# Performance work log

Hardware: AMD Instinct MI355X
Metric: run time of the kernel (lower is better)

## Reference

```python
import jax, jax.numpy as jnp
import numpy as np

B, G, CIN, COUT = 1024, 64, 512, 512  # G = s**(num_layers-1) = 2**6


def setup_inputs() -> dict:
    key = jax.random.key(0)
    kx, kw = jax.random.split(key)
    x = jax.random.normal(kx, (B, G, CIN), dtype=jnp.float32)
    weight = jax.random.normal(kw, (G, CIN, COUT), dtype=jnp.float32)
    return {"x": x, "weight": weight}


def reference(x, weight):
    # Original: (x[:,:,:,None] * W[None]).sum(2) / sqrt(Cin), then sum over groups.
    # Fused equivalent: grouped contraction over (g, c) -> [B, Cout].
    scale = 1.0 / jnp.sqrt(jnp.asarray(x.shape[2], dtype=x.dtype))
    out = jnp.einsum("bgc,gco->bo", x, weight) * scale
    return out
```

## Files before the change

kernel.cpp:

```cpp
#include <hip/hip_runtime.h>
#include <hip/hip_bf16.h>

typedef __bf16 bf16x8 __attribute__((ext_vector_type(8)));
typedef __bf16 bf16x4 __attribute__((ext_vector_type(4)));
typedef float  f32x4  __attribute__((ext_vector_type(4)));

#define B_SZ    1024
#define COUT_SZ 512
#define K_SZ    32768
#define TM 256
#define TN 256
#define BK 32

__device__ __forceinline__ void async_copy16(const void* g, void* l) {
  __builtin_amdgcn_global_load_lds(
      (const __attribute__((address_space(1))) unsigned int*)g,
      (__attribute__((address_space(3))) unsigned int*)l, 16, 0, 0);
}

__global__ __launch_bounds__(256) void wtrans_kernel(
    const float* __restrict__ w, __bf16* __restrict__ wt) {
  __shared__ float t[64 * 65];
  const int kb = blockIdx.x * 64;
  const int ob = blockIdx.y * 64;
  const int tid = threadIdx.x;

  {
    const int o4 = (tid & 15) * 4;
    const int kr = tid >> 4;
    const float* src = w + (size_t)(kb + kr) * COUT_SZ + ob + o4;
#pragma unroll
    for (int i = 0; i < 4; ++i) {
      f32x4 v = *(const f32x4*)(src + (size_t)(16 * i) * COUT_SZ);
      *(f32x4*)&t[(kr + 16 * i) * 65 + o4] = v;
    }
  }
  __syncthreads();
  {
    const int k4 = (tid & 15) * 4;
    const int orow = tid >> 4;
#pragma unroll
    for (int j = 0; j < 4; ++j) {
      const int o = orow + 16 * j;
      bf16x4 p;
#pragma unroll
      for (int e = 0; e < 4; ++e) p[e] = (__bf16)t[(k4 + e) * 65 + o];
      *(bf16x4*)(wt + (size_t)(ob + o) * K_SZ + kb + k4) = p;
    }
  }
}

__global__ __launch_bounds__(512, 2)
void gemm_kernel(const float* __restrict__ x, const __bf16* __restrict__ wt,
                 float* __restrict__ dst, int kchunk, int S) {
  __shared__ float  Asm[2][TM * BK];
  __shared__ __bf16 Bsm[2][TN * BK];

  const int lin = blockIdx.x;
  const int z = lin % S;
  const int t = lin / S;
  const int m0 = (t & 3) * TM;
  const int n0 = (t >> 2) * TN;
  const int tid  = threadIdx.x;
  const int w    = tid >> 6;
  const int lane = tid & 63;

  const int kbase = z * kchunk;

  const int aRow = lane >> 3;
  const int aCh  = (lane & 7) ^ aRow;
  const float* ag0 = x + (size_t)(m0 + (w * 4 + 0) * 8 + aRow) * K_SZ + kbase + aCh * 4;
  const float* ag1 = x + (size_t)(m0 + (w * 4 + 1) * 8 + aRow) * K_SZ + kbase + aCh * 4;
  const float* ag2 = x + (size_t)(m0 + (w * 4 + 2) * 8 + aRow) * K_SZ + kbase + aCh * 4;
  const float* ag3 = x + (size_t)(m0 + (w * 4 + 3) * 8 + aRow) * K_SZ + kbase + aCh * 4;
  const int bRow = lane >> 2;
  const int bCh  = (lane & 3) ^ ((lane >> 3) & 3);
  const __bf16* bg0 = wt + (size_t)(n0 + (w * 2 + 0) * 16 + bRow) * K_SZ + kbase + bCh * 8;
  const __bf16* bg1 = wt + (size_t)(n0 + (w * 2 + 1) * 16 + bRow) * K_SZ + kbase + bCh * 8;

  const int lm = lane & 15;
  const int q  = lane >> 4;
  const int wm = (w & 1) * 128;
  const int wn = (w >> 1) * 64;
  const int aPcLo = (2 * q) ^ (lm & 7);
  const int bPc   = q ^ ((lm >> 1) & 3);

  f32x4 acc[8][4];
#pragma unroll
  for (int i = 0; i < 8; ++i)
#pragma unroll
    for (int j = 0; j < 4; ++j)
      acc[i][j] = (f32x4){0.f, 0.f, 0.f, 0.f};

  async_copy16(ag0, &Asm[0][(w * 4 + 0) * 256]);
  async_copy16(ag1, &Asm[0][(w * 4 + 1) * 256]);
  async_copy16(ag2, &Asm[0][(w * 4 + 2) * 256]);
  async_copy16(ag3, &Asm[0][(w * 4 + 3) * 256]);
  async_copy16(bg0, &Bsm[0][(w * 2 + 0) * 512]);
  async_copy16(bg1, &Bsm[0][(w * 2 + 1) * 512]);
  ag0 += BK; ag1 += BK; ag2 += BK; ag3 += BK; bg0 += BK; bg1 += BK;

  const int niter = kchunk / BK;
  for (int it = 0; it < niter; ++it) {
    __syncthreads();
    const int p = it & 1;
    if (it + 1 < niter) {
      const int np = p ^ 1;
      async_copy16(ag0, &Asm[np][(w * 4 + 0) * 256]);
      async_copy16(ag1, &Asm[np][(w * 4 + 1) * 256]);
      async_copy16(ag2, &Asm[np][(w * 4 + 2) * 256]);
      async_copy16(ag3, &Asm[np][(w * 4 + 3) * 256]);
      async_copy16(bg0, &Bsm[np][(w * 2 + 0) * 512]);
      async_copy16(bg1, &Bsm[np][(w * 2 + 1) * 512]);
      ag0 += BK; ag1 += BK; ag2 += BK; ag3 += BK; bg0 += BK; bg1 += BK;
    }

    const float*  A_ = Asm[p];
    const __bf16* B_ = Bsm[p];
    bf16x8 bfr[4];
#pragma unroll
    for (int j = 0; j < 4; ++j)
      bfr[j] = *(const bf16x8*)&B_[(wn + j * 16 + lm) * BK + bPc * 8];

#pragma unroll
    for (int i = 0; i < 8; ++i) {
      const float* rowp = &A_[(wm + i * 16 + lm) * BK];
      f32x4 lo = *(const f32x4*)(rowp + aPcLo * 4);
      f32x4 hi = *(const f32x4*)(rowp + (aPcLo ^ 1) * 4);
      bf16x8 a;
#pragma unroll
      for (int e = 0; e < 4; ++e) {
        a[e]     = (__bf16)lo[e];
        a[e + 4] = (__bf16)hi[e];
      }
#pragma unroll
      for (int j = 0; j < 4; ++j)
        acc[i][j] = __builtin_amdgcn_mfma_f32_16x16x32_bf16(a, bfr[j], acc[i][j], 0, 0, 0);
    }
  }

  float* outp = dst + (size_t)z * (B_SZ * COUT_SZ)
              + (size_t)(m0 + wm + q * 4) * COUT_SZ + (n0 + wn + lm);
#pragma unroll
  for (int i = 0; i < 8; ++i) {
#pragma unroll
    for (int r = 0; r < 4; ++r) {
      float* o2 = outp + (size_t)(i * 16 + r) * COUT_SZ;
#pragma unroll
      for (int j = 0; j < 4; ++j)
        o2[j * 16] = acc[i][j][r];
    }
  }
}

__global__ __launch_bounds__(256) void reduce_kernel(
    const float* __restrict__ p, float* __restrict__ out, int S, float scale) {
  const int i = (blockIdx.x * 256 + threadIdx.x) * 4;
  f32x4 s0 = (f32x4){0.f, 0.f, 0.f, 0.f};
  f32x4 s1 = (f32x4){0.f, 0.f, 0.f, 0.f};
  int zz = 0;
  for (; zz + 1 < S; zz += 2) {
    s0 = s0 + *(const f32x4*)(p + (size_t)zz * (B_SZ * COUT_SZ) + i);
    s1 = s1 + *(const f32x4*)(p + (size_t)(zz + 1) * (B_SZ * COUT_SZ) + i);
  }
  for (; zz < S; ++zz)
    s0 = s0 + *(const f32x4*)(p + (size_t)zz * (B_SZ * COUT_SZ) + i);
  s0 = (s0 + s1) * scale;
  *(f32x4*)(out + i) = s0;
}

extern "C" void kernel_launch(void* const* d_in, const int* in_sizes, int n_in,
                              void* d_out, int out_size, void* d_ws, size_t ws_size,
                              hipStream_t stream) {
  const float* x = (const float*)d_in[0];
  const float* w = (const float*)d_in[1];
  float* out = (float*)d_out;

  const size_t wtB    = (size_t)COUT_SZ * K_SZ * sizeof(__bf16);
  const size_t sliceB = (size_t)B_SZ * COUT_SZ * sizeof(float);

  __bf16* wt = (__bf16*)d_ws;
  int S = 32;
  while (S > 1 && wtB + (size_t)S * sliceB > ws_size) S >>= 1;
  float* partials = (float*)((char*)d_ws + wtB);

  const float scale = 0.04419417382415922f;

  hipLaunchKernelGGL(wtrans_kernel, dim3(K_SZ / 64, COUT_SZ / 64), dim3(256), 0,
                     stream, w, wt);
  hipLaunchKernelGGL(gemm_kernel, dim3(8 * S), dim3(512), 0, stream,
                     x, wt, partials, K_SZ / S, S);
  hipLaunchKernelGGL(reduce_kernel, dim3(B_SZ * COUT_SZ / 1024), dim3(256), 0,
                     stream, partials, out, S, scale);
}
```

Baseline: 302.2 us.

## Pre-convert x to bf16 and use smaller single-buffered GEMM tiles

```diff
diff --git a/kernel.cpp b/kernel.cpp
--- a/kernel.cpp
+++ b/kernel.cpp
@@ -8,8 +8,8 @@
 #define B_SZ    1024
 #define COUT_SZ 512
 #define K_SZ    32768
-#define TM 256
-#define TN 256
+#define TM 128
+#define TN 128
 #define BK 32
 
 __device__ __forceinline__ void async_copy16(const void* g, void* l) {
@@ -18,13 +18,30 @@
       (__attribute__((address_space(3))) unsigned int*)l, 16, 0, 0);
 }
 
-__global__ __launch_bounds__(256) void wtrans_kernel(
+#define XCVT_BLOCKS 16384
+
+__global__ __launch_bounds__(256) void prep_kernel(
+    const float* __restrict__ x, __bf16* __restrict__ xb,
     const float* __restrict__ w, __bf16* __restrict__ wt) {
   __shared__ float t[64 * 65];
-  const int kb = blockIdx.x * 64;
-  const int ob = blockIdx.y * 64;
+  int b = blockIdx.x;
+  if (b < XCVT_BLOCKS) {
+    const size_t i = ((size_t)b * 256 + threadIdx.x) * 8;
+    f32x4 a = *(const f32x4*)(x + i);
+    f32x4 c = *(const f32x4*)(x + i + 4);
+    bf16x8 o;
+#pragma unroll
+    for (int e = 0; e < 4; ++e) {
+      o[e]     = (__bf16)a[e];
+      o[e + 4] = (__bf16)c[e];
+    }
+    *(bf16x8*)(xb + i) = o;
+    return;
+  }
+  b -= XCVT_BLOCKS;
+  const int kb = (b & 511) * 64;
+  const int ob = (b >> 9) * 64;
   const int tid = threadIdx.x;
-
   {
     const int o4 = (tid & 15) * 4;
     const int kr = tid >> 4;
@@ -50,99 +67,76 @@
   }
 }
 
-__global__ __launch_bounds__(512, 2)
-void gemm_kernel(const float* __restrict__ x, const __bf16* __restrict__ wt,
+__global__ __launch_bounds__(256, 3)
+void gemm_kernel(const __bf16* __restrict__ xb, const __bf16* __restrict__ wt,
                  float* __restrict__ dst, int kchunk, int S) {
-  __shared__ float  Asm[2][TM * BK];
-  __shared__ __bf16 Bsm[2][TN * BK];
+  __shared__ __bf16 As[TM * BK];
+  __shared__ __bf16 Bs[TN * BK];
 
   const int lin = blockIdx.x;
   const int z = lin % S;
   const int t = lin / S;
-  const int m0 = (t & 3) * TM;
-  const int n0 = (t >> 2) * TN;
+  const int m0 = (t & 7) * TM;
+  const int n0 = (t >> 3) * TN;
   const int tid  = threadIdx.x;
   const int w    = tid >> 6;
   const int lane = tid & 63;
-
   const int kbase = z * kchunk;
 
-  const int aRow = lane >> 3;
-  const int aCh  = (lane & 7) ^ aRow;
-  const float* ag0 = x + (size_t)(m0 + (w * 4 + 0) * 8 + aRow) * K_SZ + kbase + aCh * 4;
-  const float* ag1 = x + (size_t)(m0 + (w * 4 + 1) * 8 + aRow) * K_SZ + kbase + aCh * 4;
-  const float* ag2 = x + (size_t)(m0 + (w * 4 + 2) * 8 + aRow) * K_SZ + kbase + aCh * 4;
-  const float* ag3 = x + (size_t)(m0 + (w * 4 + 3) * 8 + aRow) * K_SZ + kbase + aCh * 4;
-  const int bRow = lane >> 2;
-  const int bCh  = (lane & 3) ^ ((lane >> 3) & 3);
-  const __bf16* bg0 = wt + (size_t)(n0 + (w * 2 + 0) * 16 + bRow) * K_SZ + kbase + bCh * 8;
-  const __bf16* bg1 = wt + (size_t)(n0 + (w * 2 + 1) * 16 + bRow) * K_SZ + kbase + bCh * 8;
+  const int sRow = lane >> 2;
+  const int sCh  = (lane & 3) ^ (sRow & 3);
+  const __bf16* ag0 = xb + (size_t)(m0 + w * 32 + sRow) * K_SZ + kbase + sCh * 8;
+  const __bf16* ag1 = xb + (size_t)(m0 + w * 32 + 16 + sRow) * K_SZ + kbase + sCh * 8;
+  const __bf16* bg0 = wt + (size_t)(n0 + w * 32 + sRow) * K_SZ + kbase + sCh * 8;
+  const __bf16* bg1 = wt + (size_t)(n0 + w * 32 + 16 + sRow) * K_SZ + kbase + sCh * 8;
+  __bf16* aL0 = &As[(w * 32) * BK];
+  __bf16* aL1 = &As[(w * 32 + 16) * BK];
+  __bf16* bL0 = &Bs[(w * 32) * BK];
+  __bf16* bL1 = &Bs[(w * 32 + 16) * BK];
 
   const int lm = lane & 15;
   const int q  = lane >> 4;
-  const int wm = (w & 1) * 128;
+  const int wm = (w & 1) * 64;
   const int wn = (w >> 1) * 64;
-  const int aPcLo = (2 * q) ^ (lm & 7);
-  const int bPc   = q ^ ((lm >> 1) & 3);
+  const int pc = q ^ (lm & 3);
 
-  f32x4 acc[8][4];
+  f32x4 acc[4][4];
 #pragma unroll
-  for (int i = 0; i < 8; ++i)
+  for (int i = 0; i < 4; ++i)
 #pragma unroll
     for (int j = 0; j < 4; ++j)
       acc[i][j] = (f32x4){0.f, 0.f, 0.f, 0.f};
 
-  async_copy16(ag0, &Asm[0][(w * 4 + 0) * 256]);
-  async_copy16(ag1, &Asm[0][(w * 4 + 1) * 256]);
-  async_copy16(ag2, &Asm[0][(w * 4 + 2) * 256]);
-  async_copy16(ag3, &Asm[0][(w * 4 + 3) * 256]);
-  async_copy16(bg0, &Bsm[0][(w * 2 + 0) * 512]);
-  async_copy16(bg1, &Bsm[0][(w * 2 + 1) * 512]);
-  ag0 += BK; ag1 += BK; ag2 += BK; ag3 += BK; bg0 += BK; bg1 += BK;
-
   const int niter = kchunk / BK;
   for (int it = 0; it < niter; ++it) {
+    async_copy16(ag0, aL0);
+    async_copy16(ag1, aL1);
+    async_copy16(bg0, bL0);
+    async_copy16(bg1, bL1);
+    ag0 += BK; ag1 += BK; bg0 += BK; bg1 += BK;
     __syncthreads();
-    const int p = it & 1;
-    if (it + 1 < niter) {
-      const int np = p ^ 1;
-      async_copy16(ag0, &Asm[np][(w * 4 + 0) * 256]);
-      async_copy16(ag1, &Asm[np][(w * 4 + 1) * 256]);
-      async_copy16(ag2, &Asm[np][(w * 4 + 2) * 256]);
-      async_copy16(ag3, &Asm[np][(w * 4 + 3) * 256]);
-      async_copy16(bg0, &Bsm[np][(w * 2 + 0) * 512]);
-      async_copy16(bg1, &Bsm[np][(w * 2 + 1) * 512]);
-      ag0 += BK; ag1 += BK; ag2 += BK; ag3 += BK; bg0 += BK; bg1 += BK;
-    }
 
-    const float*  A_ = Asm[p];
-    const __bf16* B_ = Bsm[p];
-    bf16x8 bfr[4];
+    bf16x8 af[4], bfr[4];
+#pragma unroll
+    for (int i = 0; i < 4; ++i)
+      af[i] = *(const bf16x8*)&As[(wm + i * 16 + lm) * BK + pc * 8];
 #pragma unroll
     for (int j = 0; j < 4; ++j)
-      bfr[j] = *(const bf16x8*)&B_[(wn + j * 16 + lm) * BK + bPc * 8];
+      bfr[j] = *(const bf16x8*)&Bs[(wn + j * 16 + lm) * BK + pc * 8];
 
 #pragma unroll
-    for (int i = 0; i < 8; ++i) {
-      const float* rowp = &A_[(wm + i * 16 + lm) * BK];
-      f32x4 lo = *(const f32x4*)(rowp + aPcLo * 4);
-      f32x4 hi = *(const f32x4*)(rowp + (aPcLo ^ 1) * 4);
-      bf16x8 a;
-#pragma unroll
-      for (int e = 0; e < 4; ++e) {
-        a[e]     = (__bf16)lo[e];
-        a[e + 4] = (__bf16)hi[e];
-      }
+    for (int i = 0; i < 4; ++i)
 #pragma unroll
       for (int j = 0; j < 4; ++j)
-        acc[i][j] = __builtin_amdgcn_mfma_f32_16x16x32_bf16(a, bfr[j], acc[i][j], 0, 0, 0);
-    }
+        acc[i][j] = __builtin_amdgcn_mfma_f32_16x16x32_bf16(af[i], bfr[j], acc[i][j], 0, 0, 0);
+
+    __syncthreads();
   }
 
   float* outp = dst + (size_t)z * (B_SZ * COUT_SZ)
               + (size_t)(m0 + wm + q * 4) * COUT_SZ + (n0 + wn + lm);
 #pragma unroll
-  for (int i = 0; i < 8; ++i) {
+  for (int i = 0; i < 4; ++i) {
 #pragma unroll
     for (int r = 0; r < 4; ++r) {
       float* o2 = outp + (size_t)(i * 16 + r) * COUT_SZ;
@@ -177,19 +171,23 @@
   float* out = (float*)d_out;
 
   const size_t wtB    = (size_t)COUT_SZ * K_SZ * sizeof(__bf16);
+  const size_t xbB    = (size_t)B_SZ * K_SZ * sizeof(__bf16);
   const size_t sliceB = (size_t)B_SZ * COUT_SZ * sizeof(float);
 
   __bf16* wt = (__bf16*)d_ws;
+  __bf16* xb = (__bf16*)((char*)d_ws + wtB);
+  float* partials = (float*)((char*)d_ws + wtB + xbB);
+
   int S = 32;
-  while (S > 1 && wtB + (size_t)S * sliceB > ws_size) S >>= 1;
-  float* partials = (float*)((char*)d_ws + wtB);
+  while (S > 1 && wtB + xbB + (size_t)S * sliceB > ws_size) S >>= 1;
+  if (wtB + xbB + sliceB > ws_size) { partials = out; S = 1; }
 
   const float scale = 0.04419417382415922f;
 
-  hipLaunchKernelGGL(wtrans_kernel, dim3(K_SZ / 64, COUT_SZ / 64), dim3(256), 0,
-                     stream, w, wt);
-  hipLaunchKernelGGL(gemm_kernel, dim3(8 * S), dim3(512), 0, stream,
-                     x, wt, partials, K_SZ / S, S);
+  hipLaunchKernelGGL(prep_kernel, dim3(XCVT_BLOCKS + (K_SZ / 64) * (COUT_SZ / 64)),
+                     dim3(256), 0, stream, x, xb, w, wt);
+  hipLaunchKernelGGL(gemm_kernel, dim3(32 * S), dim3(256), 0, stream,
+                     xb, wt, partials, K_SZ / S, S);
   hipLaunchKernelGGL(reduce_kernel, dim3(B_SZ * COUT_SZ / 1024), dim3(256), 0,
                      stream, partials, out, S, scale);
 }
```

New measurement: 320.1 us. +5.9%, slower.
